# Kernel optimization log

Hardware: AMD Instinct MI355X
Metric: run time of the kernel (lower is better)

## Reference

```python
import jax, jax.numpy as jnp
import numpy as np

T, B, E = 512, 128, 256  # timesteps, batch_size, embedding_size


def setup_inputs() -> dict:
    key = jax.random.key(0)
    k1, k2, k3 = jax.random.split(key, 3)
    return {
        "v": jax.random.normal(k1, (T, B, E), dtype=jnp.float32),
        "u": jax.random.uniform(k2, (T, B), dtype=jnp.float32),  # pop signals in (0,1)
        "d": jax.random.uniform(k3, (T, B), dtype=jnp.float32),  # push signals in (0,1)
    }


def _pop(s, w):
    """Grefenstette-stack pop: s [T,B] strengths (stack grows along dim 0,
    padded with zeros past the current depth), w [B] pop amount.
    Reverse cumsum, subtract w, clamp at 0, then difference to recover per-slot
    strengths. Zero padding at the tail is preserved exactly (contributes 0)."""
    top = jnp.cumsum(s[::-1], axis=0) - w[None, :]
    top = jnp.clip(top, 0.0)
    top = top - jnp.concatenate([jnp.zeros_like(top[:1]), top[:-1]], axis=0)
    return top[::-1]


def reference(v, u, d):
    # v: [T, B, E] pushed vectors; u, d: [T, B] pop/push strengths.
    T_, B_ = u.shape
    E_ = v.shape[-1]
    ones = jnp.ones((B_,), v.dtype)

    def step(carry, xs):
        V, s = carry  # V: [T,B,E] value buffer, s: [T,B] strengths (zero-padded)
        t, v_t, u_t, d_t = xs
        V = V.at[t].set(v_t)
        # forward(): pop with u (original detaches s and u inside pop), then push d
        s = _pop(jax.lax.stop_gradient(s), jax.lax.stop_gradient(u_t)).at[t].set(d_t)
        # read(): weights = s - pop(s, 1); r = sum_t weights * V
        weights = s - _pop(jax.lax.stop_gradient(s), ones)
        r = jnp.einsum('tb,tbe->be', weights, V)
        return (V, s), r

    init = (jnp.zeros((T_, B_, E_), v.dtype), jnp.zeros((T_, B_), v.dtype))
    _, rs = jax.lax.scan(step, init, (jnp.arange(T_), v, u, d))
    return rs  # [T, B, E] read vector at each timestep
```

## Files before the change

### kernel.cpp

```cpp
#include <hip/hip_runtime.h>

#define T_DIM 512
#define B_DIM 128
#define E_DIM 256
#define L_CAP 16
#define NEG_INF (-1e30f)


struct Node { float g; int ngl; };

__global__ void __launch_bounds__(512) scan_prep(
    const float* __restrict__ u, const float* __restrict__ d,
    Node* __restrict__ nodes, float2* __restrict__ lists, int4* __restrict__ aux)
{
    const int b    = blockIdx.x;
    const int t    = threadIdx.x;
    const int lane = t & 63;
    const int w    = t >> 6;

    __shared__ float wsum[8];
    __shared__ float wpre[8];
    __shared__ float M[10][T_DIM];
    __shared__ int   ngl_s[T_DIM];
    __shared__ float2 stage[T_DIM * L_CAP];

    const float dv = d[t * B_DIM + b];
    float x = dv - u[t * B_DIM + b];

    #pragma unroll
    for (int off = 1; off < 64; off <<= 1) {
        float y = __shfl_up(x, off, 64);
        if (lane >= off) x += y;
    }
    if (lane == 63) wsum[w] = x;
    __syncthreads();
    if (t < 8) {
        float s = 0.f;
        for (int i = 0; i < t; ++i) s += wsum[i];
        wpre[t] = s;
    }
    __syncthreads();
    const float S = x + wpre[w];
    const float g = dv - S;

    M[0][t] = g;
    __syncthreads();
    #pragma unroll
    for (int k = 1; k < 10; ++k) {
        int h = 1 << (k - 1);
        float left = (t >= h) ? M[k - 1][t - h] : NEG_INF;
        float mk = fmaxf(M[k - 1][t], left);
        __syncthreads();
        M[k][t] = mk;
        __syncthreads();
    }

    int m = t - 1;
    #pragma unroll
    for (int k = 9; k >= 0; --k) {
        if (m >= 0 && M[k][m] <= g) m -= (1 << k);
    }
    if (m < 0) m = -1;
    ngl_s[t] = m;
    nodes[(b << 9) | t] = Node{g, m};
    __syncthreads();

    float2* mystage = &stage[t * L_CAP];
    float prev = 0.f;
    int mcur = t, cnt = 0, tailm = -1;
    float tailprev = 0.f;
    #pragma unroll 1
    for (;;) {
        float gm = M[0][mcur];
        float rc = S + gm;
        float cur = fminf(rc, 1.f);
        mystage[cnt] = make_float2(cur - prev, __int_as_float(mcur));
        ++cnt; prev = cur;
        int nx = ngl_s[mcur];
        if (rc >= 1.f || nx < 0) break;
        if (cnt == L_CAP) { tailm = nx; tailprev = prev; break; }
        mcur = nx;
    }
    aux[(b << 9) | t] = make_int4(cnt, tailm, __float_as_int(tailprev), __float_as_int(S));
    __syncthreads();

    float4* gl = (float4*)(lists + (size_t)(b << 9) * L_CAP);
    const float4* st = (const float4*)stage;
    #pragma unroll
    for (int i = 0; i < (T_DIM * L_CAP) / 2 / 512; ++i)
        gl[i * 512 + t] = st[i * 512 + t];
}

__global__ void __launch_bounds__(256) stack_read(
    const float* __restrict__ v, const Node* __restrict__ nodes,
    const float2* __restrict__ lists, const int4* __restrict__ aux,
    float* __restrict__ out)
{
    const int wid  = (blockIdx.x << 2) | (threadIdx.x >> 6);
    const int lane = threadIdx.x & 63;
    const int b = wid >> 9;
    const int t = wid & 511;
    const int e4 = lane << 2;
    const float* __restrict__ vb = v + (size_t)b * E_DIM + e4;

    const int4 ax = aux[wid];
    const int cnt = ax.x;

    float2 pr = lists[(size_t)wid * L_CAP + (lane & 15)];
    float my_w = pr.x;
    int   my_m = __float_as_int(pr.y);

    float4 acc = {0.f, 0.f, 0.f, 0.f};
    const int nc = (cnt + 3) >> 2;
    #pragma unroll 1
    for (int c = 0; c < nc; ++c) {
        float wj[4]; float4 vj[4];
        #pragma unroll
        for (int j = 0; j < 4; ++j) {
            int idx = (c << 2) + j;
            int   mj = __shfl(my_m, idx, 64);
            float ww = __shfl(my_w, idx, 64);
            bool on = idx < cnt;
            mj = on ? mj : t;
            wj[j] = on ? ww : 0.f;
            vj[j] = *(const float4*)(vb + (size_t)mj * (B_DIM * E_DIM));
        }
        #pragma unroll
        for (int j = 0; j < 4; ++j) {
            acc.x += wj[j] * vj[j].x; acc.y += wj[j] * vj[j].y;
            acc.z += wj[j] * vj[j].z; acc.w += wj[j] * vj[j].w;
        }
    }

    if (ax.y >= 0) {
        const float S = __int_as_float(ax.w);
        float prev = __int_as_float(ax.z);
        int m = ax.y;
        const Node* __restrict__ nb = nodes + (b << 9);
        while (true) {
            Node nd = nb[m];
            float rc = S + nd.g;
            float cur = fminf(rc, 1.f);
            float ww = cur - prev;
            float4 vv = *(const float4*)(vb + (size_t)m * (B_DIM * E_DIM));
            acc.x += ww * vv.x; acc.y += ww * vv.y;
            acc.z += ww * vv.z; acc.w += ww * vv.w;
            prev = cur;
            if (rc >= 1.f || nd.ngl < 0) break;
            m = nd.ngl;
        }
    }

    *(float4*)(out + ((size_t)t * B_DIM + b) * E_DIM + e4) = acc;
}

extern "C" void kernel_launch(void* const* d_in, const int* in_sizes, int n_in,
                              void* d_out, int out_size, void* d_ws, size_t ws_size,
                              hipStream_t stream) {
    const float* v = (const float*)d_in[0];
    const float* u = (const float*)d_in[1];
    const float* d = (const float*)d_in[2];
    float* out = (float*)d_out;

    char* ws = (char*)d_ws;
    Node*   node = (Node*)ws;
    float2* list = (float2*)(ws + (1 << 19));
    int4*   aux  = (int4*)(ws + (1 << 19) + (1 << 23));

    scan_prep<<<dim3(B_DIM), 512, 0, stream>>>(u, d, node, list, aux);
    stack_read<<<dim3((T_DIM * B_DIM) / 4), 256, 0, stream>>>(v, node, list, aux, out);
}
```

Before: 139.7 us.

## Split read work across two waves per row and batch gathers unrolled

Each (t,b) output row is now handled by two wavefronts, each covering half the embedding with float2 loads, which doubles the number of waves and the latency hiding available. The list gather loop is fully unrolled so up to 16 loads are issued before any accumulation. Unused list slots are padded with zero weight and self index, so the masking is dropped. Block indices are remapped with an XCD-style swizzle to change how work spreads across dies. The cost is narrower loads per lane and duplicate list and aux reads for each half.

```diff
diff --git a/kernel.cpp b/kernel.cpp
--- a/kernel.cpp
+++ b/kernel.cpp
@@ -81,6 +81,8 @@
         if (cnt == L_CAP) { tailm = nx; tailprev = prev; break; }
         mcur = nx;
     }
+    for (int i = cnt; i < L_CAP; ++i)
+        mystage[i] = make_float2(0.f, __int_as_float(t));
     aux[(b << 9) | t] = make_int4(cnt, tailm, __float_as_int(tailprev), __float_as_int(S));
     __syncthreads();
 
@@ -96,39 +98,47 @@
     const float2* __restrict__ lists, const int4* __restrict__ aux,
     float* __restrict__ out)
 {
-    const int wid  = (blockIdx.x << 2) | (threadIdx.x >> 6);
+    const int lb   = ((blockIdx.x & 7) << 12) | (blockIdx.x >> 3);
+    const int wid2 = (lb << 2) | (threadIdx.x >> 6);
     const int lane = threadIdx.x & 63;
-    const int b = wid >> 9;
-    const int t = wid & 511;
-    const int e4 = lane << 2;
-    const float* __restrict__ vb = v + (size_t)b * E_DIM + e4;
+    const int eh   = wid2 & 1;
+    const int tb   = wid2 >> 1;
+    const int b    = tb >> 9;
+    const int t    = tb & 511;
+    const int eo   = (eh << 7) | (lane << 1);
 
-    const int4 ax = aux[wid];
-    const int cnt = ax.x;
+    const float* __restrict__ vb = v + (size_t)b * E_DIM + eo;
 
-    float2 pr = lists[(size_t)wid * L_CAP + (lane & 15)];
+    const int4 ax = aux[tb];
+    float2 pr = lists[(size_t)tb * L_CAP + (lane & 15)];
     float my_w = pr.x;
     int   my_m = __float_as_int(pr.y);
+    const int nc = (ax.x + 3) >> 2;
 
-    float4 acc = {0.f, 0.f, 0.f, 0.f};
-    const int nc = (cnt + 3) >> 2;
-    #pragma unroll 1
-    for (int c = 0; c < nc; ++c) {
-        float wj[4]; float4 vj[4];
-        #pragma unroll
-        for (int j = 0; j < 4; ++j) {
-            int idx = (c << 2) + j;
-            int   mj = __shfl(my_m, idx, 64);
-            float ww = __shfl(my_w, idx, 64);
-            bool on = idx < cnt;
-            mj = on ? mj : t;
-            wj[j] = on ? ww : 0.f;
-            vj[j] = *(const float4*)(vb + (size_t)mj * (B_DIM * E_DIM));
+    float2 vj[16]; float wj[16];
+    #pragma unroll
+    for (int c = 0; c < 4; ++c) {
+        if (c < nc) {
+            #pragma unroll
+            for (int j = 0; j < 4; ++j) {
+                const int idx = (c << 2) + j;
+                int   mj = __shfl(my_m, idx, 64);
+                float ww = __shfl(my_w, idx, 64);
+                wj[idx] = ww;
+                vj[idx] = *(const float2*)(vb + (size_t)mj * (B_DIM * E_DIM));
+            }
         }
-        #pragma unroll
-        for (int j = 0; j < 4; ++j) {
-            acc.x += wj[j] * vj[j].x; acc.y += wj[j] * vj[j].y;
-            acc.z += wj[j] * vj[j].z; acc.w += wj[j] * vj[j].w;
+    }
+    float2 acc = {0.f, 0.f};
+    #pragma unroll
+    for (int c = 0; c < 4; ++c) {
+        if (c < nc) {
+            #pragma unroll
+            for (int j = 0; j < 4; ++j) {
+                const int idx = (c << 2) + j;
+                acc.x += wj[idx] * vj[idx].x;
+                acc.y += wj[idx] * vj[idx].y;
+            }
         }
     }
 
@@ -142,16 +152,15 @@
             float rc = S + nd.g;
             float cur = fminf(rc, 1.f);
             float ww = cur - prev;
-            float4 vv = *(const float4*)(vb + (size_t)m * (B_DIM * E_DIM));
+            float2 vv = *(const float2*)(vb + (size_t)m * (B_DIM * E_DIM));
             acc.x += ww * vv.x; acc.y += ww * vv.y;
-            acc.z += ww * vv.z; acc.w += ww * vv.w;
             prev = cur;
             if (rc >= 1.f || nd.ngl < 0) break;
             m = nd.ngl;
         }
     }
 
-    *(float4*)(out + ((size_t)t * B_DIM + b) * E_DIM + e4) = acc;
+    *(float2*)(out + ((size_t)t * B_DIM + b) * E_DIM + eo) = acc;
 }
 
 extern "C" void kernel_launch(void* const* d_in, const int* in_sizes, int n_in,
@@ -168,5 +177,5 @@
     int4*   aux  = (int4*)(ws + (1 << 19) + (1 << 23));
 
     scan_prep<<<dim3(B_DIM), 512, 0, stream>>>(u, d, node, list, aux);
-    stack_read<<<dim3((T_DIM * B_DIM) / 4), 256, 0, stream>>>(v, node, list, aux, out);
+    stack_read<<<dim3((T_DIM * B_DIM * 2) / 4), 256, 0, stream>>>(v, node, list, aux, out);
 }
```

Result: slower. 157.1 us (+12.5%).
